# Kernel tuning notes

Hardware: AMD Instinct MI355X
Metric: run time of the kernel (lower is better)

## Reference

```python
import jax, jax.numpy as jnp
import numpy as np

B, D, H, E, TOPK = 65536, 1024, 512, 8, 2
LN_EPS = 1e-5
LB_WEIGHT = 0.01


def setup_inputs() -> dict:
    key = jax.random.key(0)
    ks = jax.random.split(key, 5)
    x = jax.random.normal(ks[0], (B, D), dtype=jnp.float32)
    W1 = jax.random.normal(ks[1], (D, H), dtype=jnp.float32) * 0.02
    b1 = jnp.zeros((H,), dtype=jnp.float32)
    ln_w = jnp.ones((H,), dtype=jnp.float32)
    ln_b = jnp.zeros((H,), dtype=jnp.float32)
    W2 = jax.random.normal(ks[2], (H, E), dtype=jnp.float32) * 0.02
    b2 = jnp.zeros((E,), dtype=jnp.float32)
    return {"x": x, "W1": W1, "b1": b1, "ln_w": ln_w, "ln_b": ln_b, "W2": W2, "b2": b2}


def _gate_logits(x, W1, b1, ln_w, ln_b, W2, b2):
    h = x @ W1 + b1                     # [B, H]
    mu = jnp.mean(h, axis=-1, keepdims=True)
    var = jnp.mean(jnp.square(h - mu), axis=-1, keepdims=True)
    h = (h - mu) * jax.lax.rsqrt(var + LN_EPS) * ln_w + ln_b
    h = jax.nn.gelu(h, approximate=False)  # torch nn.GELU default = exact erf
    return h @ W2 + b2                  # [B, E]


def reference(x, W1, b1, ln_w, ln_b, W2, b2):
    logits = _gate_logits(x, W1, b1, ln_w, ln_b, W2, b2)
    # sparse top-K routing (eval mode: no exploration noise)
    vals, idx = jax.lax.top_k(logits, TOPK)           # [B, K]
    rows = jnp.arange(logits.shape[0])[:, None]
    sparse = jnp.full_like(logits, -jnp.inf).at[rows, idx].set(vals)
    weights = jax.nn.softmax(sparse, axis=-1)         # zeros off top-k
    # Switch-style load-balance loss
    f = (weights > 0).astype(weights.dtype).mean(axis=0)  # fraction routed per expert
    P = weights.mean(axis=0)                              # mean gate prob per expert
    lb_loss = LB_WEIGHT * (E * jnp.sum(f * P))
    return weights, lb_loss
```

## Files before the change

kernel.cpp:

```cpp
#include <hip/hip_runtime.h>
#include <cstdint>
#include <cstddef>


typedef _Float16 f16;
typedef _Float16 f16x4 __attribute__((ext_vector_type(4)));
typedef _Float16 f16x8 __attribute__((ext_vector_type(8)));
typedef float f32x4 __attribute__((ext_vector_type(4)));

#define B_ROWS 65536
#define D_DIM 1024
#define H_DIM 512
#define E_DIM 8
#define BM 64
#define BK 32
#define THREADS 512
#define NCHUNK 32
#define LDPX 40
#define SLABH 2560
#define BUFH 5120
#define IMG_CH (H_DIM * BK)
#define IMG_TOTAL (32 * IMG_CH)
#define GACC_OFF ((size_t)2 * IMG_TOTAL * sizeof(f16))

__global__ void prep_split(const float* __restrict__ W1,
                           f16* __restrict__ wh, f16* __restrict__ wl) {
  int id = blockIdx.x * 256 + threadIdx.x;
  int h = id & (H_DIM - 1);
  int kg = id >> 9;
  int c = kg >> 2;
  int kk0 = (kg & 3) * 8;
  int k0 = kg * 8;
  f16x8 hv, lv;
#pragma unroll
  for (int j = 0; j < 8; ++j) {
    float v = W1[(size_t)(k0 + j) * H_DIM + h] * 64.0f;
    f16 hi = (f16)v;
    hv[j] = hi;
    lv[j] = (f16)((v - (float)hi) * 256.0f);
  }
  size_t o = (size_t)c * IMG_CH + (size_t)h * BK + kk0;
  *(f16x8*)&wh[o] = hv;
  *(f16x8*)&wl[o] = lv;
}

__global__ void zero_acc(float* __restrict__ acc) {
  if (threadIdx.x < 16) acc[threadIdx.x] = 0.0f;
}

__global__ __launch_bounds__(THREADS, 4) void fused_main(
    const float* __restrict__ x,
    const f16* __restrict__ wh, const f16* __restrict__ wl,
    const float* __restrict__ b1, const float* __restrict__ lnw,
    const float* __restrict__ lnb, const float* __restrict__ W2,
    const float* __restrict__ b2, float* __restrict__ out,
    float* __restrict__ gacc) {
  __shared__ __align__(16) char pool[45632];
  f16* sx = (f16*)pool;

  const int tid = threadIdx.x;
  const int lane = tid & 63;
  const int wv = tid >> 6;
  const int l15 = lane & 15;
  const int l4 = lane >> 4;
  const int64_t row0 = (int64_t)blockIdx.x * BM;

  const int srow = tid >> 3;
  const int sc4 = (tid & 7) * 4;
  const int swo = srow * LDPX + sc4;
  const float* xbase = x + (row0 + srow) * D_DIM + sc4;

  const f16* whp = wh + (wv * 64 + l15) * BK + l4 * 8;

  f32x4 acc[4][4];
#pragma unroll
  for (int m = 0; m < 4; ++m)
#pragma unroll
    for (int n = 0; n < 4; ++n) acc[m][n] = (f32x4){0.f, 0.f, 0.f, 0.f};

  f16x8 setB[2][4];

#define ISSUE(si, C, half)                                                    \
  do {                                                                        \
    const f16* p = whp + (size_t)((C) & 31) * IMG_CH + (half) * 1024;         \
    setB[si][0] = *(const f16x8*)(p);                                         \
    setB[si][1] = *(const f16x8*)(p + 512);                                   \
    setB[si][2] = *(const f16x8*)(p + IMG_TOTAL);                             \
    setB[si][3] = *(const f16x8*)(p + IMG_TOTAL + 512);                       \
  } while (0)

#define CHUNK_HALF(si, nh, bufv)                                              \
  do {                                                                        \
    __builtin_amdgcn_s_setprio(1);                                            \
    _Pragma("unroll") for (int m = 0; m < 4; ++m) {                           \
      const int ao = (bufv)*BUFH + (m * 16 + l15) * LDPX + l4 * 8;            \
      f16x8 ah = *(const f16x8*)&sx[ao];                                      \
      f16x8 al = *(const f16x8*)&sx[ao + SLABH];                              \
      f16x8 ahs;                                                              \
      _Pragma("unroll") for (int q = 0; q < 8; ++q) ahs[q] =                  \
          ah[q] * (f16)0.00390625f;                                           \
      acc[m][(nh)*2 + 0] = __builtin_amdgcn_mfma_f32_16x16x32_f16(            \
          ah, setB[si][0], acc[m][(nh)*2 + 0], 0, 0, 0);                      \
      acc[m][(nh)*2 + 0] = __builtin_amdgcn_mfma_f32_16x16x32_f16(            \
          al, setB[si][0], acc[m][(nh)*2 + 0], 0, 0, 0);                      \
      acc[m][(nh)*2 + 0] = __builtin_amdgcn_mfma_f32_16x16x32_f16(            \
          ahs, setB[si][2], acc[m][(nh)*2 + 0], 0, 0, 0);                     \
      acc[m][(nh)*2 + 1] = __builtin_amdgcn_mfma_f32_16x16x32_f16(            \
          ah, setB[si][1], acc[m][(nh)*2 + 1], 0, 0, 0);                      \
      acc[m][(nh)*2 + 1] = __builtin_amdgcn_mfma_f32_16x16x32_f16(            \
          al, setB[si][1], acc[m][(nh)*2 + 1], 0, 0, 0);                      \
      acc[m][(nh)*2 + 1] = __builtin_amdgcn_mfma_f32_16x16x32_f16(            \
          ahs, setB[si][3], acc[m][(nh)*2 + 1], 0, 0, 0);                     \
    }                                                                         \
    __builtin_amdgcn_s_setprio(0);                                            \
  } while (0)

#define WRITE_SLAB(bufv)                                                      \
  do {                                                                        \
    float vv[4] = {xv.x, xv.y, xv.z, xv.w};                                   \
    f16x4 hv, lv;                                                             \
    _Pragma("unroll") for (int q = 0; q < 4; ++q) {                           \
      float t = vv[q] * 64.0f;                                                \
      f16 hh = (f16)t;                                                        \
      hv[q] = hh;                                                             \
      lv[q] = (f16)(t - (float)hh);                                           \
    }                                                                         \
    *(f16x4*)&sx[(bufv)*BUFH + swo] = hv;                                     \
    *(f16x4*)&sx[(bufv)*BUFH + SLABH + swo] = lv;                             \
  } while (0)

#define SLAB_BARRIER()                                                        \
  do {                                                                        \
    asm volatile("s_waitcnt lgkmcnt(0)" ::: "memory");                        \
    __builtin_amdgcn_s_barrier();                                             \
    __builtin_amdgcn_sched_barrier(0);                                        \
  } while (0)

  float4 xv = *(const float4*)(xbase);
  WRITE_SLAB(0);
  ISSUE(0, 0, 0);
  ISSUE(1, 0, 1);
  xv = *(const float4*)(xbase + 32);
  SLAB_BARRIER();

  for (int c = 0; c < NCHUNK; ++c) {
    const int buf = c & 1;
    CHUNK_HALF(0, 0, buf);
    ISSUE(0, c + 1, 0);
    CHUNK_HALF(1, 1, buf);
    ISSUE(1, c + 1, 1);
    WRITE_SLAB(buf ^ 1);
    xv = *(const float4*)(xbase + ((c + 2) & 31) * 32);
    SLAB_BARRIER();
  }
#undef ISSUE
#undef CHUNK_HALF
#undef WRITE_SLAB
#undef SLAB_BARRIER
  __syncthreads();

  float* eW2T = (float*)pool;
  float* eStat = (float*)(pool + 24576);
  float* eLog = (float*)(pool + 28672);
  float* eMu = (float*)(pool + 45056);
  float* eRs = (float*)(pool + 45312);
  float* eFP = (float*)(pool + 45568);

  {
    float4 wa = *(const float4*)&W2[tid * 8];
    float4 wb = *(const float4*)&W2[tid * 8 + 4];
    *(float4*)&eW2T[tid * 12] = wa;
    *(float4*)&eW2T[tid * 12 + 4] = wb;
  }
  if (tid < 16) eFP[tid] = 0.0f;

  float bb[4], lw[4], lb[4];
#pragma unroll
  for (int n = 0; n < 4; ++n) {
    int col = wv * 64 + n * 16 + l15;
    bb[n] = b1[col] * 4096.0f;
    lw[n] = lnw[col];
    lb[n] = lnb[col];
#pragma unroll
    for (int m = 0; m < 4; ++m)
#pragma unroll
      for (int r = 0; r < 4; ++r) acc[m][n][r] += bb[n];
  }

#pragma unroll
  for (int m = 0; m < 4; ++m) {
    float s1[4] = {0, 0, 0, 0};
    float s2[4] = {0, 0, 0, 0};
#pragma unroll
    for (int n = 0; n < 4; ++n)
#pragma unroll
      for (int r = 0; r < 4; ++r) {
        float vv = acc[m][n][r];
        s1[r] += vv;
        s2[r] = fmaf(vv, vv, s2[r]);
      }
#pragma unroll
    for (int d = 1; d < 16; d <<= 1)
#pragma unroll
      for (int r = 0; r < 4; ++r) {
        s1[r] += __shfl_xor(s1[r], d);
        s2[r] += __shfl_xor(s2[r], d);
      }
    if (l15 == 0) {
      int rb = m * 16 + l4 * 4;
#pragma unroll
      for (int r = 0; r < 4; ++r) {
        eStat[(wv * 64 + rb + r) * 2 + 0] = s1[r];
        eStat[(wv * 64 + rb + r) * 2 + 1] = s2[r];
      }
    }
  }
  __syncthreads();
  if (tid < BM) {
    float s1 = 0.0f, s2 = 0.0f;
#pragma unroll
    for (int w = 0; w < 8; ++w) {
      s1 += eStat[(w * 64 + tid) * 2 + 0];
      s2 += eStat[(w * 64 + tid) * 2 + 1];
    }
    float mu = s1 * (1.0f / 512.0f);
    float var = s2 * (1.0f / 512.0f) - mu * mu;
    eMu[tid] = mu;
    eRs[tid] = 1.0f / sqrtf(var + (1e-5f * 4096.0f * 4096.0f));
  }
  __syncthreads();

#pragma unroll
  for (int m = 0; m < 4; ++m) {
    int rb = m * 16 + l4 * 4;
#pragma unroll
    for (int r = 0; r < 4; ++r) {
      float mu_r = eMu[rb + r];
      float rs_r = eRs[rb + r];
      float lg[8];
#pragma unroll
      for (int e = 0; e < 8; ++e) lg[e] = 0.0f;
#pragma unroll
      for (int n = 0; n < 4; ++n) {
        int col = wv * 64 + n * 16 + l15;
        float hn = (acc[m][n][r] - mu_r) * rs_r;
        float y = fmaf(hn, lw[n], lb[n]);
        float g = 0.5f * y * (1.0f + erff(y * 0.70710678118654752440f));
        float4 w0 = *(const float4*)&eW2T[col * 12];
        float4 w1 = *(const float4*)&eW2T[col * 12 + 4];
        lg[0] = fmaf(g, w0.x, lg[0]);
        lg[1] = fmaf(g, w0.y, lg[1]);
        lg[2] = fmaf(g, w0.z, lg[2]);
        lg[3] = fmaf(g, w0.w, lg[3]);
        lg[4] = fmaf(g, w1.x, lg[4]);
        lg[5] = fmaf(g, w1.y, lg[5]);
        lg[6] = fmaf(g, w1.z, lg[6]);
        lg[7] = fmaf(g, w1.w, lg[7]);
      }
#pragma unroll
      for (int d = 1; d < 16; d <<= 1)
#pragma unroll
        for (int e = 0; e < 8; ++e) lg[e] += __shfl_xor(lg[e], d);
      if (l15 == 0) {
#pragma unroll
        for (int e = 0; e < 8; ++e) eLog[(wv * 64 + rb + r) * 8 + e] = lg[e];
      }
    }
  }
  __syncthreads();

  if (tid < BM) {
    float v[8];
#pragma unroll
    for (int e = 0; e < 8; ++e) {
      float s = b2[e];
#pragma unroll
      for (int w = 0; w < 8; ++w) s += eLog[(w * 64 + tid) * 8 + e];
      v[e] = s;
    }
    float m1 = v[0];
    int i1 = 0;
#pragma unroll
    for (int e = 1; e < 8; ++e)
      if (v[e] > m1) { m1 = v[e]; i1 = e; }
    float m2 = -3.0e38f;
    int i2 = -1;
#pragma unroll
    for (int e = 0; e < 8; ++e)
      if (e != i1 && v[e] > m2) { m2 = v[e]; i2 = e; }
    float dd = expf(m2 - m1);
    float inv = 1.0f / (1.0f + dd);
    float wA = inv, wB = dd * inv;
    float o[8];
#pragma unroll
    for (int e = 0; e < 8; ++e)
      o[e] = (e == i1) ? wA : ((e == i2) ? wB : 0.0f);
    float4* op = (float4*)&out[(row0 + tid) * 8];
    op[0] = (float4){o[0], o[1], o[2], o[3]};
    op[1] = (float4){o[4], o[5], o[6], o[7]};
    atomicAdd(&eFP[i1], 1.0f);
    atomicAdd(&eFP[i2], 1.0f);
    atomicAdd(&eFP[8 + i1], wA);
    atomicAdd(&eFP[8 + i2], wB);
  }
  __syncthreads();
  if (tid < 16) atomicAdd(&gacc[tid], eFP[tid]);
}

__global__ void lb_final(const float* __restrict__ gacc, float* __restrict__ out) {
  if (threadIdx.x == 0) {
    const float invB = 1.0f / 65536.0f;
    float s = 0.0f;
#pragma unroll
    for (int e = 0; e < 8; ++e) s += (gacc[e] * invB) * (gacc[8 + e] * invB);
    out[(size_t)B_ROWS * E_DIM] = 0.01f * 8.0f * s;
  }
}

extern "C" void kernel_launch(void* const* d_in, const int* in_sizes, int n_in,
                              void* d_out, int out_size, void* d_ws, size_t ws_size,
                              hipStream_t stream) {
  (void)in_sizes; (void)n_in; (void)out_size; (void)ws_size;
  const float* x = (const float*)d_in[0];
  const float* W1 = (const float*)d_in[1];
  const float* b1 = (const float*)d_in[2];
  const float* lnw = (const float*)d_in[3];
  const float* lnb = (const float*)d_in[4];
  const float* W2 = (const float*)d_in[5];
  const float* b2 = (const float*)d_in[6];
  float* out = (float*)d_out;
  f16* wh = (f16*)d_ws;
  f16* wl = wh + IMG_TOTAL;
  float* gacc = (float*)((char*)d_ws + GACC_OFF);

  zero_acc<<<1, 64, 0, stream>>>(gacc);
  prep_split<<<(D_DIM * H_DIM / 8) / 256, 256, 0, stream>>>(W1, wh, wl);
  fused_main<<<B_ROWS / BM, THREADS, 0, stream>>>(x, wh, wl, b1, lnw, lnb, W2, b2,
                                                  out, gacc);
  lb_final<<<1, 64, 0, stream>>>(gacc, out);
}
```

Before: 249.7 us.

## Switch GEMM to 32x32x16 MFMA tiles with matching weight layout and epilogue

Replaces the 16x16x32 MFMA tiling with 32x32x16 MFMA instructions, so each wave holds 2x2 accumulator tiles of 16 floats. The weight image is re-laid out in K-steps of 16, and each 32-wide chunk is split into two k-steps. The epilogue is rewritten for the new accumulator row and column mapping, and it keeps W2 in registers instead of staging it in LDS, which shrinks LDS use. The goal is fewer MFMA and operand-load instructions per FLOP and higher occupancy from the smaller LDS footprint. In exchange, the epilogue needs longer 32-lane shuffle reductions.

```diff
diff --git a/kernel.cpp b/kernel.cpp
--- a/kernel.cpp
+++ b/kernel.cpp
@@ -6,7 +6,7 @@
 typedef _Float16 f16;
 typedef _Float16 f16x4 __attribute__((ext_vector_type(4)));
 typedef _Float16 f16x8 __attribute__((ext_vector_type(8)));
-typedef float f32x4 __attribute__((ext_vector_type(4)));
+typedef float f32x16 __attribute__((ext_vector_type(16)));
 
 #define B_ROWS 65536
 #define D_DIM 1024
@@ -19,8 +19,8 @@
 #define LDPX 40
 #define SLABH 2560
 #define BUFH 5120
-#define IMG_CH (H_DIM * BK)
-#define IMG_TOTAL (32 * IMG_CH)
+#define STEPH (H_DIM * 16)
+#define IMG_TOTAL (64 * STEPH)
 #define GACC_OFF ((size_t)2 * IMG_TOTAL * sizeof(f16))
 
 __global__ void prep_split(const float* __restrict__ W1,
@@ -28,9 +28,9 @@
   int id = blockIdx.x * 256 + threadIdx.x;
   int h = id & (H_DIM - 1);
   int kg = id >> 9;
-  int c = kg >> 2;
-  int kk0 = (kg & 3) * 8;
   int k0 = kg * 8;
+  int s = k0 >> 4;
+  int ko = k0 & 15;
   f16x8 hv, lv;
 #pragma unroll
   for (int j = 0; j < 8; ++j) {
@@ -39,7 +39,7 @@
     hv[j] = hi;
     lv[j] = (f16)((v - (float)hi) * 256.0f);
   }
-  size_t o = (size_t)c * IMG_CH + (size_t)h * BK + kk0;
+  size_t o = (size_t)s * STEPH + (size_t)h * 16 + ko;
   *(f16x8*)&wh[o] = hv;
   *(f16x8*)&wl[o] = lv;
 }
@@ -55,14 +55,14 @@
     const float* __restrict__ lnb, const float* __restrict__ W2,
     const float* __restrict__ b2, float* __restrict__ out,
     float* __restrict__ gacc) {
-  __shared__ __align__(16) char pool[45632];
+  __shared__ __align__(16) char pool[21056];
   f16* sx = (f16*)pool;
 
   const int tid = threadIdx.x;
   const int lane = tid & 63;
   const int wv = tid >> 6;
-  const int l15 = lane & 15;
-  const int l4 = lane >> 4;
+  const int l31 = lane & 31;
+  const int hi5 = lane >> 5;
   const int64_t row0 = (int64_t)blockIdx.x * BM;
 
   const int srow = tid >> 3;
@@ -70,47 +70,50 @@
   const int swo = srow * LDPX + sc4;
   const float* xbase = x + (row0 + srow) * D_DIM + sc4;
 
-  const f16* whp = wh + (wv * 64 + l15) * BK + l4 * 8;
-
-  f32x4 acc[4][4];
-#pragma unroll
-  for (int m = 0; m < 4; ++m)
-#pragma unroll
-    for (int n = 0; n < 4; ++n) acc[m][n] = (f32x4){0.f, 0.f, 0.f, 0.f};
+  const int blane = (wv * 64 + l31) * 16 + hi5 * 8;
+  const f16* whp = wh + blane;
+
+  f32x16 acc[2][2];
+#pragma unroll
+  for (int mt = 0; mt < 2; ++mt)
+#pragma unroll
+    for (int nt = 0; nt < 2; ++nt)
+#pragma unroll
+      for (int r = 0; r < 16; ++r) acc[mt][nt][r] = 0.0f;
 
   f16x8 setB[2][4];
 
-#define ISSUE(si, C, half)                                                    \
+#define ISSUE(si, G)                                                          \
   do {                                                                        \
-    const f16* p = whp + (size_t)((C) & 31) * IMG_CH + (half) * 1024;         \
+    const f16* p = whp + (size_t)((G) & 63) * STEPH;                          \
     setB[si][0] = *(const f16x8*)(p);                                         \
     setB[si][1] = *(const f16x8*)(p + 512);                                   \
     setB[si][2] = *(const f16x8*)(p + IMG_TOTAL);                             \
     setB[si][3] = *(const f16x8*)(p + IMG_TOTAL + 512);                       \
   } while (0)
 
-#define CHUNK_HALF(si, nh, bufv)                                              \
+#define KSTEP(si, ks, bufv)                                                   \
   do {                                                                        \
     __builtin_amdgcn_s_setprio(1);                                            \
-    _Pragma("unroll") for (int m = 0; m < 4; ++m) {                           \
-      const int ao = (bufv)*BUFH + (m * 16 + l15) * LDPX + l4 * 8;            \
+    _Pragma("unroll") for (int mt = 0; mt < 2; ++mt) {                        \
+      const int ao = (bufv)*BUFH + (mt * 32 + l31) * LDPX + (ks)*16 + hi5 * 8;\
       f16x8 ah = *(const f16x8*)&sx[ao];                                      \
       f16x8 al = *(const f16x8*)&sx[ao + SLABH];                              \
       f16x8 ahs;                                                              \
       _Pragma("unroll") for (int q = 0; q < 8; ++q) ahs[q] =                  \
           ah[q] * (f16)0.00390625f;                                           \
-      acc[m][(nh)*2 + 0] = __builtin_amdgcn_mfma_f32_16x16x32_f16(            \
-          ah, setB[si][0], acc[m][(nh)*2 + 0], 0, 0, 0);                      \
-      acc[m][(nh)*2 + 0] = __builtin_amdgcn_mfma_f32_16x16x32_f16(            \
-          al, setB[si][0], acc[m][(nh)*2 + 0], 0, 0, 0);                      \
-      acc[m][(nh)*2 + 0] = __builtin_amdgcn_mfma_f32_16x16x32_f16(            \
-          ahs, setB[si][2], acc[m][(nh)*2 + 0], 0, 0, 0);                     \
-      acc[m][(nh)*2 + 1] = __builtin_amdgcn_mfma_f32_16x16x32_f16(            \
-          ah, setB[si][1], acc[m][(nh)*2 + 1], 0, 0, 0);                      \
-      acc[m][(nh)*2 + 1] = __builtin_amdgcn_mfma_f32_16x16x32_f16(            \
-          al, setB[si][1], acc[m][(nh)*2 + 1], 0, 0, 0);                      \
-      acc[m][(nh)*2 + 1] = __builtin_amdgcn_mfma_f32_16x16x32_f16(            \
-          ahs, setB[si][3], acc[m][(nh)*2 + 1], 0, 0, 0);                     \
+      acc[mt][0] = __builtin_amdgcn_mfma_f32_32x32x16_f16(                    \
+          ah, setB[si][0], acc[mt][0], 0, 0, 0);                              \
+      acc[mt][0] = __builtin_amdgcn_mfma_f32_32x32x16_f16(                    \
+          al, setB[si][0], acc[mt][0], 0, 0, 0);                              \
+      acc[mt][0] = __builtin_amdgcn_mfma_f32_32x32x16_f16(                    \
+          ahs, setB[si][2], acc[mt][0], 0, 0, 0);                             \
+      acc[mt][1] = __builtin_amdgcn_mfma_f32_32x32x16_f16(                    \
+          ah, setB[si][1], acc[mt][1], 0, 0, 0);                              \
+      acc[mt][1] = __builtin_amdgcn_mfma_f32_32x32x16_f16(                    \
+          al, setB[si][1], acc[mt][1], 0, 0, 0);                              \
+      acc[mt][1] = __builtin_amdgcn_mfma_f32_32x32x16_f16(                    \
+          ahs, setB[si][3], acc[mt][1], 0, 0, 0);                             \
     }                                                                         \
     __builtin_amdgcn_s_setprio(0);                                            \
   } while (0)
@@ -138,83 +141,81 @@
 
   float4 xv = *(const float4*)(xbase);
   WRITE_SLAB(0);
-  ISSUE(0, 0, 0);
-  ISSUE(1, 0, 1);
+  ISSUE(0, 0);
+  ISSUE(1, 1);
   xv = *(const float4*)(xbase + 32);
   SLAB_BARRIER();
 
   for (int c = 0; c < NCHUNK; ++c) {
     const int buf = c & 1;
-    CHUNK_HALF(0, 0, buf);
-    ISSUE(0, c + 1, 0);
-    CHUNK_HALF(1, 1, buf);
-    ISSUE(1, c + 1, 1);
+    KSTEP(0, 0, buf);
+    ISSUE(0, 2 * c + 2);
+    KSTEP(1, 1, buf);
+    ISSUE(1, 2 * c + 3);
     WRITE_SLAB(buf ^ 1);
     xv = *(const float4*)(xbase + ((c + 2) & 31) * 32);
     SLAB_BARRIER();
   }
 #undef ISSUE
-#undef CHUNK_HALF
+#undef KSTEP
 #undef WRITE_SLAB
 #undef SLAB_BARRIER
   __syncthreads();
 
-  float* eW2T = (float*)pool;
-  float* eStat = (float*)(pool + 24576);
-  float* eLog = (float*)(pool + 28672);
-  float* eMu = (float*)(pool + 45056);
-  float* eRs = (float*)(pool + 45312);
-  float* eFP = (float*)(pool + 45568);
-
-  {
-    float4 wa = *(const float4*)&W2[tid * 8];
-    float4 wb = *(const float4*)&W2[tid * 8 + 4];
-    *(float4*)&eW2T[tid * 12] = wa;
-    *(float4*)&eW2T[tid * 12 + 4] = wb;
+  float* eStat = (float*)pool;
+  float* eLog = (float*)(pool + 4096);
+  float* eMu = (float*)(pool + 20480);
+  float* eRs = (float*)(pool + 20736);
+  float* eFP = (float*)(pool + 20992);
+
+  float bb[2], lw[2], lb[2];
+  float4 w2a[2], w2b[2];
+#pragma unroll
+  for (int nt = 0; nt < 2; ++nt) {
+    int col = wv * 64 + nt * 32 + l31;
+    bb[nt] = b1[col] * 4096.0f;
+    lw[nt] = lnw[col];
+    lb[nt] = lnb[col];
+    w2a[nt] = *(const float4*)&W2[col * 8];
+    w2b[nt] = *(const float4*)&W2[col * 8 + 4];
   }
   if (tid < 16) eFP[tid] = 0.0f;
 
-  float bb[4], lw[4], lb[4];
-#pragma unroll
-  for (int n = 0; n < 4; ++n) {
-    int col = wv * 64 + n * 16 + l15;
-    bb[n] = b1[col] * 4096.0f;
-    lw[n] = lnw[col];
-    lb[n] = lnb[col];
-#pragma unroll
-    for (int m = 0; m < 4; ++m)
-#pragma unroll
-      for (int r = 0; r < 4; ++r) acc[m][n][r] += bb[n];
-  }
-
-#pragma unroll
-  for (int m = 0; m < 4; ++m) {
-    float s1[4] = {0, 0, 0, 0};
-    float s2[4] = {0, 0, 0, 0};
-#pragma unroll
-    for (int n = 0; n < 4; ++n)
+#pragma unroll
+  for (int mt = 0; mt < 2; ++mt)
+#pragma unroll
+    for (int nt = 0; nt < 2; ++nt)
+#pragma unroll
+      for (int r = 0; r < 16; ++r) acc[mt][nt][r] += bb[nt];
+
+#pragma unroll
+  for (int mt = 0; mt < 2; ++mt)
+#pragma unroll
+    for (int q = 0; q < 4; ++q) {
+      float s1[4], s2[4];
 #pragma unroll
       for (int r = 0; r < 4; ++r) {
-        float vv = acc[m][n][r];
-        s1[r] += vv;
-        s2[r] = fmaf(vv, vv, s2[r]);
+        float v0 = acc[mt][0][q * 4 + r];
+        float v1 = acc[mt][1][q * 4 + r];
+        s1[r] = v0 + v1;
+        s2[r] = fmaf(v0, v0, v1 * v1);
       }
 #pragma unroll
-    for (int d = 1; d < 16; d <<= 1)
-#pragma unroll
-      for (int r = 0; r < 4; ++r) {
-        s1[r] += __shfl_xor(s1[r], d);
-        s2[r] += __shfl_xor(s2[r], d);
-      }
-    if (l15 == 0) {
-      int rb = m * 16 + l4 * 4;
-#pragma unroll
-      for (int r = 0; r < 4; ++r) {
-        eStat[(wv * 64 + rb + r) * 2 + 0] = s1[r];
-        eStat[(wv * 64 + rb + r) * 2 + 1] = s2[r];
+      for (int d = 1; d < 32; d <<= 1)
+#pragma unroll
+        for (int r = 0; r < 4; ++r) {
+          s1[r] += __shfl_xor(s1[r], d);
+          s2[r] += __shfl_xor(s2[r], d);
+        }
+      if (l31 == 0) {
+        int rb = 8 * q + 4 * hi5 + 32 * mt;
+#pragma unroll
+        for (int r = 0; r < 4; ++r) {
+          eStat[(wv * 64 + rb + r) * 2 + 0] = s1[r];
+          eStat[(wv * 64 + rb + r) * 2 + 1] = s2[r];
+        }
       }
     }
-  }
   __syncthreads();
   if (tid < BM) {
     float s1 = 0.0f, s2 = 0.0f;
@@ -231,42 +232,41 @@
   __syncthreads();
 
 #pragma unroll
-  for (int m = 0; m < 4; ++m) {
-    int rb = m * 16 + l4 * 4;
-#pragma unroll
-    for (int r = 0; r < 4; ++r) {
-      float mu_r = eMu[rb + r];
-      float rs_r = eRs[rb + r];
-      float lg[8];
-#pragma unroll
-      for (int e = 0; e < 8; ++e) lg[e] = 0.0f;
-#pragma unroll
-      for (int n = 0; n < 4; ++n) {
-        int col = wv * 64 + n * 16 + l15;
-        float hn = (acc[m][n][r] - mu_r) * rs_r;
-        float y = fmaf(hn, lw[n], lb[n]);
-        float g = 0.5f * y * (1.0f + erff(y * 0.70710678118654752440f));
-        float4 w0 = *(const float4*)&eW2T[col * 12];
-        float4 w1 = *(const float4*)&eW2T[col * 12 + 4];
-        lg[0] = fmaf(g, w0.x, lg[0]);
-        lg[1] = fmaf(g, w0.y, lg[1]);
-        lg[2] = fmaf(g, w0.z, lg[2]);
-        lg[3] = fmaf(g, w0.w, lg[3]);
-        lg[4] = fmaf(g, w1.x, lg[4]);
-        lg[5] = fmaf(g, w1.y, lg[5]);
-        lg[6] = fmaf(g, w1.z, lg[6]);
-        lg[7] = fmaf(g, w1.w, lg[7]);
+  for (int mt = 0; mt < 2; ++mt)
+#pragma unroll
+    for (int q = 0; q < 4; ++q)
+#pragma unroll
+      for (int r = 0; r < 4; ++r) {
+        const int reg = q * 4 + r;
+        const int row = r + 8 * q + 4 * hi5 + 32 * mt;
+        float mu_r = eMu[row];
+        float rs_r = eRs[row];
+        float lg[8];
+#pragma unroll
+        for (int e = 0; e < 8; ++e) lg[e] = 0.0f;
+#pragma unroll
+        for (int nt = 0; nt < 2; ++nt) {
+          float hn = (acc[mt][nt][reg] - mu_r) * rs_r;
+          float y = fmaf(hn, lw[nt], lb[nt]);
+          float g = 0.5f * y * (1.0f + erff(y * 0.70710678118654752440f));
+          lg[0] = fmaf(g, w2a[nt].x, lg[0]);
+          lg[1] = fmaf(g, w2a[nt].y, lg[1]);
+          lg[2] = fmaf(g, w2a[nt].z, lg[2]);
+          lg[3] = fmaf(g, w2a[nt].w, lg[3]);
+          lg[4] = fmaf(g, w2b[nt].x, lg[4]);
+          lg[5] = fmaf(g, w2b[nt].y, lg[5]);
+          lg[6] = fmaf(g, w2b[nt].z, lg[6]);
+          lg[7] = fmaf(g, w2b[nt].w, lg[7]);
+        }
+#pragma unroll
+        for (int d = 1; d < 32; d <<= 1)
+#pragma unroll
+          for (int e = 0; e < 8; ++e) lg[e] += __shfl_xor(lg[e], d);
+        if (l31 == 0) {
+#pragma unroll
+          for (int e = 0; e < 8; ++e) eLog[(wv * 64 + row) * 8 + e] = lg[e];
+        }
       }
-#pragma unroll
-      for (int d = 1; d < 16; d <<= 1)
-#pragma unroll
-        for (int e = 0; e < 8; ++e) lg[e] += __shfl_xor(lg[e], d);
-      if (l15 == 0) {
-#pragma unroll
-        for (int e = 0; e < 8; ++e) eLog[(wv * 64 + rb + r) * 8 + e] = lg[e];
-      }
-    }
-  }
   __syncthreads();
 
   if (tid < BM) {
```

Result: slower. 315.1 us (+26.2%).

## Stage 64-wide K super-chunks in LDS to halve barriers per K loop

Applied to the files above, without the earlier changes.

Each shared-memory slab now holds 64 K columns instead of 32. Each thread loads two float4s and writes 8-wide f16 hi/lo vectors, and the main loop runs 16 super-iterations of two 32-wide sub-chunks, so the barrier and slab-write overhead is paid half as often. The MFMA sequence is also interleaved across the two accumulators to ease dependency stalls. The cost is more LDS per block (padded stride 72), which may lower occupancy under the 4-block launch bound, and the weight register prefetch still advances per 32-chunk.

```diff
diff --git a/kernel.cpp b/kernel.cpp
--- a/kernel.cpp
+++ b/kernel.cpp
@@ -4,7 +4,6 @@
 
 
 typedef _Float16 f16;
-typedef _Float16 f16x4 __attribute__((ext_vector_type(4)));
 typedef _Float16 f16x8 __attribute__((ext_vector_type(8)));
 typedef float f32x4 __attribute__((ext_vector_type(4)));
 
@@ -15,10 +14,10 @@
 #define BM 64
 #define BK 32
 #define THREADS 512
-#define NCHUNK 32
-#define LDPX 40
-#define SLABH 2560
-#define BUFH 5120
+#define NSUPER 16
+#define LDPX 72
+#define SLABH 4608
+#define BUFH 9216
 #define IMG_CH (H_DIM * BK)
 #define IMG_TOTAL (32 * IMG_CH)
 #define GACC_OFF ((size_t)2 * IMG_TOTAL * sizeof(f16))
@@ -66,9 +65,9 @@
   const int64_t row0 = (int64_t)blockIdx.x * BM;
 
   const int srow = tid >> 3;
-  const int sc4 = (tid & 7) * 4;
-  const int swo = srow * LDPX + sc4;
-  const float* xbase = x + (row0 + srow) * D_DIM + sc4;
+  const int sk = (tid & 7) * 8;
+  const int swo = srow * LDPX + sk;
+  const float* xbase = x + (row0 + srow) * D_DIM + sk;
 
   const f16* whp = wh + (wv * 64 + l15) * BK + l4 * 8;
 
@@ -89,11 +88,11 @@
     setB[si][3] = *(const f16x8*)(p + IMG_TOTAL + 512);                       \
   } while (0)
 
-#define CHUNK_HALF(si, nh, bufv)                                              \
+#define CHUNK_HALF(si, nh, ch, bufv)                                          \
   do {                                                                        \
     __builtin_amdgcn_s_setprio(1);                                            \
     _Pragma("unroll") for (int m = 0; m < 4; ++m) {                           \
-      const int ao = (bufv)*BUFH + (m * 16 + l15) * LDPX + l4 * 8;            \
+      const int ao = (bufv)*BUFH + (m * 16 + l15) * LDPX + (ch)*32 + l4 * 8;  \
       f16x8 ah = *(const f16x8*)&sx[ao];                                      \
       f16x8 al = *(const f16x8*)&sx[ao + SLABH];                              \
       f16x8 ahs;                                                              \
@@ -101,14 +100,14 @@
           ah[q] * (f16)0.00390625f;                                           \
       acc[m][(nh)*2 + 0] = __builtin_amdgcn_mfma_f32_16x16x32_f16(            \
           ah, setB[si][0], acc[m][(nh)*2 + 0], 0, 0, 0);                      \
+      acc[m][(nh)*2 + 1] = __builtin_amdgcn_mfma_f32_16x16x32_f16(            \
+          ah, setB[si][1], acc[m][(nh)*2 + 1], 0, 0, 0);                      \
       acc[m][(nh)*2 + 0] = __builtin_amdgcn_mfma_f32_16x16x32_f16(            \
           al, setB[si][0], acc[m][(nh)*2 + 0], 0, 0, 0);                      \
+      acc[m][(nh)*2 + 1] = __builtin_amdgcn_mfma_f32_16x16x32_f16(            \
+          al, setB[si][1], acc[m][(nh)*2 + 1], 0, 0, 0);                      \
       acc[m][(nh)*2 + 0] = __builtin_amdgcn_mfma_f32_16x16x32_f16(            \
           ahs, setB[si][2], acc[m][(nh)*2 + 0], 0, 0, 0);                     \
-      acc[m][(nh)*2 + 1] = __builtin_amdgcn_mfma_f32_16x16x32_f16(            \
-          ah, setB[si][1], acc[m][(nh)*2 + 1], 0, 0, 0);                      \
-      acc[m][(nh)*2 + 1] = __builtin_amdgcn_mfma_f32_16x16x32_f16(            \
-          al, setB[si][1], acc[m][(nh)*2 + 1], 0, 0, 0);                      \
       acc[m][(nh)*2 + 1] = __builtin_amdgcn_mfma_f32_16x16x32_f16(            \
           ahs, setB[si][3], acc[m][(nh)*2 + 1], 0, 0, 0);                     \
     }                                                                         \
@@ -117,16 +116,16 @@
 
 #define WRITE_SLAB(bufv)                                                      \
   do {                                                                        \
-    float vv[4] = {xv.x, xv.y, xv.z, xv.w};                                   \
-    f16x4 hv, lv;                                                             \
-    _Pragma("unroll") for (int q = 0; q < 4; ++q) {                           \
+    float vv[8] = {xv0.x, xv0.y, xv0.z, xv0.w, xv1.x, xv1.y, xv1.z, xv1.w};   \
+    f16x8 hv, lv;                                                             \
+    _Pragma("unroll") for (int q = 0; q < 8; ++q) {                           \
       float t = vv[q] * 64.0f;                                                \
       f16 hh = (f16)t;                                                        \
       hv[q] = hh;                                                             \
       lv[q] = (f16)(t - (float)hh);                                           \
     }                                                                         \
-    *(f16x4*)&sx[(bufv)*BUFH + swo] = hv;                                     \
-    *(f16x4*)&sx[(bufv)*BUFH + SLABH + swo] = lv;                             \
+    *(f16x8*)&sx[(bufv)*BUFH + swo] = hv;                                     \
+    *(f16x8*)&sx[(bufv)*BUFH + SLABH + swo] = lv;                             \
   } while (0)
 
 #define SLAB_BARRIER()                                                        \
@@ -136,21 +135,28 @@
     __builtin_amdgcn_sched_barrier(0);                                        \
   } while (0)
 
-  float4 xv = *(const float4*)(xbase);
+  float4 xv0 = *(const float4*)(xbase);
+  float4 xv1 = *(const float4*)(xbase + 4);
   WRITE_SLAB(0);
   ISSUE(0, 0, 0);
   ISSUE(1, 0, 1);
-  xv = *(const float4*)(xbase + 32);
+  xv0 = *(const float4*)(xbase + 64);
+  xv1 = *(const float4*)(xbase + 68);
   SLAB_BARRIER();
 
-  for (int c = 0; c < NCHUNK; ++c) {
-    const int buf = c & 1;
-    CHUNK_HALF(0, 0, buf);
-    ISSUE(0, c + 1, 0);
-    CHUNK_HALF(1, 1, buf);
-    ISSUE(1, c + 1, 1);
+  for (int s = 0; s < NSUPER; ++s) {
+    const int buf = s & 1;
+    CHUNK_HALF(0, 0, 0, buf);
+    ISSUE(0, 2 * s + 1, 0);
+    CHUNK_HALF(1, 1, 0, buf);
+    ISSUE(1, 2 * s + 1, 1);
+    CHUNK_HALF(0, 0, 1, buf);
+    ISSUE(0, 2 * s + 2, 0);
+    CHUNK_HALF(1, 1, 1, buf);
+    ISSUE(1, 2 * s + 2, 1);
     WRITE_SLAB(buf ^ 1);
-    xv = *(const float4*)(xbase + ((c + 2) & 31) * 32);
+    xv0 = *(const float4*)(xbase + (((s + 2) & 15) * 64));
+    xv1 = *(const float4*)(xbase + (((s + 2) & 15) * 64) + 4);
     SLAB_BARRIER();
   }
 #undef ISSUE
```

Result: no change. 248.9 us (-0.3%).

## Halve block to 4 waves, each computing 128 H columns per row tile

Applied to the files above, without the earlier changes.

The block shrinks from 8 waves to 4. Each wave now owns 128 hidden columns (8 accumulator tiles) instead of 64, so every A-fragment read from LDS feeds twice as many MFMAs and B loads are issued 8 per half-chunk. The x staging load widens to two float4s per thread, and the cross-wave reductions for LN stats and logits shrink to 4 waves. In exchange, register pressure roughly doubles (acc[4][8] plus setB[2][8]), launch bounds drop to 2 blocks, and there are fewer waves to hide global-load latency.

```diff
diff --git a/kernel.cpp b/kernel.cpp
--- a/kernel.cpp
+++ b/kernel.cpp
@@ -4,7 +4,6 @@
 
 
 typedef _Float16 f16;
-typedef _Float16 f16x4 __attribute__((ext_vector_type(4)));
 typedef _Float16 f16x8 __attribute__((ext_vector_type(8)));
 typedef float f32x4 __attribute__((ext_vector_type(4)));
 
@@ -14,7 +13,7 @@
 #define E_DIM 8
 #define BM 64
 #define BK 32
-#define THREADS 512
+#define THREADS 256
 #define NCHUNK 32
 #define LDPX 40
 #define SLABH 2560
@@ -48,14 +47,14 @@
   if (threadIdx.x < 16) acc[threadIdx.x] = 0.0f;
 }
 
-__global__ __launch_bounds__(THREADS, 4) void fused_main(
+__global__ __launch_bounds__(THREADS, 2) void fused_main(
     const float* __restrict__ x,
     const f16* __restrict__ wh, const f16* __restrict__ wl,
     const float* __restrict__ b1, const float* __restrict__ lnw,
     const float* __restrict__ lnb, const float* __restrict__ W2,
     const float* __restrict__ b2, float* __restrict__ out,
     float* __restrict__ gacc) {
-  __shared__ __align__(16) char pool[45632];
+  __shared__ __align__(16) char pool[35584];
   f16* sx = (f16*)pool;
 
   const int tid = threadIdx.x;
@@ -65,68 +64,75 @@
   const int l4 = lane >> 4;
   const int64_t row0 = (int64_t)blockIdx.x * BM;
 
-  const int srow = tid >> 3;
-  const int sc4 = (tid & 7) * 4;
-  const int swo = srow * LDPX + sc4;
-  const float* xbase = x + (row0 + srow) * D_DIM + sc4;
-
-  const f16* whp = wh + (wv * 64 + l15) * BK + l4 * 8;
-
-  f32x4 acc[4][4];
+  const int srow = tid >> 2;
+  const int koff = (tid & 3) * 8;
+  const int swo = srow * LDPX + koff;
+  const float* xbase = x + (row0 + srow) * D_DIM + koff;
+
+  const f16* whp = wh + (wv * 128 + l15) * BK + l4 * 8;
+
+  f32x4 acc[4][8];
 #pragma unroll
   for (int m = 0; m < 4; ++m)
 #pragma unroll
-    for (int n = 0; n < 4; ++n) acc[m][n] = (f32x4){0.f, 0.f, 0.f, 0.f};
-
-  f16x8 setB[2][4];
+    for (int n = 0; n < 8; ++n) acc[m][n] = (f32x4){0.f, 0.f, 0.f, 0.f};
+
+  f16x8 setB[2][8];
 
 #define ISSUE(si, C, half)                                                    \
   do {                                                                        \
-    const f16* p = whp + (size_t)((C) & 31) * IMG_CH + (half) * 1024;         \
+    const f16* p = whp + (size_t)((C) & 31) * IMG_CH + (half) * 2048;         \
     setB[si][0] = *(const f16x8*)(p);                                         \
     setB[si][1] = *(const f16x8*)(p + 512);                                   \
-    setB[si][2] = *(const f16x8*)(p + IMG_TOTAL);                             \
-    setB[si][3] = *(const f16x8*)(p + IMG_TOTAL + 512);                       \
-  } while (0)
-
-#define CHUNK_HALF(si, nh, bufv)                                              \
+    setB[si][2] = *(const f16x8*)(p + 1024);                                  \
+    setB[si][3] = *(const f16x8*)(p + 1536);                                  \
+    setB[si][4] = *(const f16x8*)(p + IMG_TOTAL);                             \
+    setB[si][5] = *(const f16x8*)(p + IMG_TOTAL + 512);                       \
+    setB[si][6] = *(const f16x8*)(p + IMG_TOTAL + 1024);                      \
+    setB[si][7] = *(const f16x8*)(p + IMG_TOTAL + 1536);                      \
+  } while (0)
+
+#define CH_M(si, NH, bufv, MM)                                                \
+  do {                                                                        \
+    const int ao = (bufv)*BUFH + ((MM)*16 + l15) * LDPX + l4 * 8;             \
+    f16x8 ah = *(const f16x8*)&sx[ao];                                        \
+    f16x8 al = *(const f16x8*)&sx[ao + SLABH];                                \
+    f16x8 ahs;                                                                \
+    _Pragma("unroll") for (int q = 0; q < 8; ++q) ahs[q] =                    \
+        ah[q] * (f16)0.00390625f;                                             \
+    _Pragma("unroll") for (int n = 0; n < 4; ++n)                             \
+      acc[MM][(NH)*4 + n] = __builtin_amdgcn_mfma_f32_16x16x32_f16(           \
+          ah, setB[si][n], acc[MM][(NH)*4 + n], 0, 0, 0);                     \
+    _Pragma("unroll") for (int n = 0; n < 4; ++n)                             \
+      acc[MM][(NH)*4 + n] = __builtin_amdgcn_mfma_f32_16x16x32_f16(           \
+          al, setB[si][n], acc[MM][(NH)*4 + n], 0, 0, 0);                     \
+    _Pragma("unroll") for (int n = 0; n < 4; ++n)                             \
+      acc[MM][(NH)*4 + n] = __builtin_amdgcn_mfma_f32_16x16x32_f16(           \
+          ahs, setB[si][4 + n], acc[MM][(NH)*4 + n], 0, 0, 0);                \
+  } while (0)
+
+#define HALF(si, NH, bufv)                                                    \
   do {                                                                        \
     __builtin_amdgcn_s_setprio(1);                                            \
-    _Pragma("unroll") for (int m = 0; m < 4; ++m) {                           \
-      const int ao = (bufv)*BUFH + (m * 16 + l15) * LDPX + l4 * 8;            \
-      f16x8 ah = *(const f16x8*)&sx[ao];                                      \
-      f16x8 al = *(const f16x8*)&sx[ao + SLABH];                              \
-      f16x8 ahs;                                                              \
-      _Pragma("unroll") for (int q = 0; q < 8; ++q) ahs[q] =                  \
-          ah[q] * (f16)0.00390625f;                                           \
-      acc[m][(nh)*2 + 0] = __builtin_amdgcn_mfma_f32_16x16x32_f16(            \
-          ah, setB[si][0], acc[m][(nh)*2 + 0], 0, 0, 0);                      \
-      acc[m][(nh)*2 + 0] = __builtin_amdgcn_mfma_f32_16x16x32_f16(            \
-          al, setB[si][0], acc[m][(nh)*2 + 0], 0, 0, 0);                      \
-      acc[m][(nh)*2 + 0] = __builtin_amdgcn_mfma_f32_16x16x32_f16(            \
-          ahs, setB[si][2], acc[m][(nh)*2 + 0], 0, 0, 0);                     \
-      acc[m][(nh)*2 + 1] = __builtin_amdgcn_mfma_f32_16x16x32_f16(            \
-          ah, setB[si][1], acc[m][(nh)*2 + 1], 0, 0, 0);                      \
-      acc[m][(nh)*2 + 1] = __builtin_amdgcn_mfma_f32_16x16x32_f16(            \
-          al, setB[si][1], acc[m][(nh)*2 + 1], 0, 0, 0);                      \
-      acc[m][(nh)*2 + 1] = __builtin_amdgcn_mfma_f32_16x16x32_f16(            \
-          ahs, setB[si][3], acc[m][(nh)*2 + 1], 0, 0, 0);                     \
-    }                                                                         \
+    CH_M(si, NH, bufv, 0);                                                    \
+    CH_M(si, NH, bufv, 1);                                                    \
+    CH_M(si, NH, bufv, 2);                                                    \
+    CH_M(si, NH, bufv, 3);                                                    \
     __builtin_amdgcn_s_setprio(0);                                            \
   } while (0)
 
 #define WRITE_SLAB(bufv)                                                      \
   do {                                                                        \
-    float vv[4] = {xv.x, xv.y, xv.z, xv.w};                                   \
-    f16x4 hv, lv;                                                             \
-    _Pragma("unroll") for (int q = 0; q < 4; ++q) {                           \
+    float vv[8] = {xv0.x, xv0.y, xv0.z, xv0.w, xv1.x, xv1.y, xv1.z, xv1.w};   \
+    f16x8 hv, lv;                                                             \
+    _Pragma("unroll") for (int q = 0; q < 8; ++q) {                           \
       float t = vv[q] * 64.0f;                                                \
       f16 hh = (f16)t;                                                        \
       hv[q] = hh;                                                             \
       lv[q] = (f16)(t - (float)hh);                                           \
     }                                                                         \
-    *(f16x4*)&sx[(bufv)*BUFH + swo] = hv;                                     \
-    *(f16x4*)&sx[(bufv)*BUFH + SLABH + swo] = lv;                             \
+    *(f16x8*)&sx[(bufv)*BUFH + swo] = hv;                                     \
+    *(f16x8*)&sx[(bufv)*BUFH + SLABH + swo] = lv;                             \
   } while (0)
 
 #define SLAB_BARRIER()                                                        \
@@ -136,48 +142,52 @@
     __builtin_amdgcn_sched_barrier(0);                                        \
   } while (0)
 
-  float4 xv = *(const float4*)(xbase);
+  float4 xv0 = *(const float4*)(xbase);
+  float4 xv1 = *(const float4*)(xbase + 4);
   WRITE_SLAB(0);
   ISSUE(0, 0, 0);
   ISSUE(1, 0, 1);
-  xv = *(const float4*)(xbase + 32);
+  xv0 = *(const float4*)(xbase + 32);
+  xv1 = *(const float4*)(xbase + 36);
   SLAB_BARRIER();
 
   for (int c = 0; c < NCHUNK; ++c) {
     const int buf = c & 1;
-    CHUNK_HALF(0, 0, buf);
+    HALF(0, 0, buf);
     ISSUE(0, c + 1, 0);
-    CHUNK_HALF(1, 1, buf);
+    HALF(1, 1, buf);
     ISSUE(1, c + 1, 1);
     WRITE_SLAB(buf ^ 1);
-    xv = *(const float4*)(xbase + ((c + 2) & 31) * 32);
+    xv0 = *(const float4*)(xbase + ((c + 2) & 31) * 32);
+    xv1 = *(const float4*)(xbase + ((c + 2) & 31) * 32 + 4);
     SLAB_BARRIER();
   }
 #undef ISSUE
-#undef CHUNK_HALF
+#undef CH_M
+#undef HALF
 #undef WRITE_SLAB
 #undef SLAB_BARRIER
   __syncthreads();
 
   float* eW2T = (float*)pool;
   float* eStat = (float*)(pool + 24576);
-  float* eLog = (float*)(pool + 28672);
-  float* eMu = (float*)(pool + 45056);
-  float* eRs = (float*)(pool + 45312);
-  float* eFP = (float*)(pool + 45568);
-
-  {
-    float4 wa = *(const float4*)&W2[tid * 8];
-    float4 wb = *(const float4*)&W2[tid * 8 + 4];
-    *(float4*)&eW2T[tid * 12] = wa;
-    *(float4*)&eW2T[tid * 12 + 4] = wb;
+  float* eLog = (float*)(pool + 26624);
+  float* eMu = (float*)(pool + 34816);
+  float* eRs = (float*)(pool + 35072);
+  float* eFP = (float*)(pool + 35328);
+
+  for (int i = tid; i < H_DIM; i += THREADS) {
+    float4 wa = *(const float4*)&W2[i * 8];
+    float4 wb = *(const float4*)&W2[i * 8 + 4];
+    *(float4*)&eW2T[i * 12] = wa;
+    *(float4*)&eW2T[i * 12 + 4] = wb;
   }
   if (tid < 16) eFP[tid] = 0.0f;
 
-  float bb[4], lw[4], lb[4];
-#pragma unroll
-  for (int n = 0; n < 4; ++n) {
-    int col = wv * 64 + n * 16 + l15;
+  float bb[8], lw[8], lb[8];
+#pragma unroll
+  for (int n = 0; n < 8; ++n) {
+    int col = wv * 128 + n * 16 + l15;
     bb[n] = b1[col] * 4096.0f;
     lw[n] = lnw[col];
     lb[n] = lnb[col];
@@ -192,7 +202,7 @@
     float s1[4] = {0, 0, 0, 0};
     float s2[4] = {0, 0, 0, 0};
 #pragma unroll
-    for (int n = 0; n < 4; ++n)
+    for (int n = 0; n < 8; ++n)
 #pragma unroll
       for (int r = 0; r < 4; ++r) {
         float vv = acc[m][n][r];
@@ -219,7 +229,7 @@
   if (tid < BM) {
     float s1 = 0.0f, s2 = 0.0f;
 #pragma unroll
-    for (int w = 0; w < 8; ++w) {
+    for (int w = 0; w < 4; ++w) {
       s1 += eStat[(w * 64 + tid) * 2 + 0];
       s2 += eStat[(w * 64 + tid) * 2 + 1];
     }
@@ -241,8 +251,8 @@
 #pragma unroll
       for (int e = 0; e < 8; ++e) lg[e] = 0.0f;
 #pragma unroll
-      for (int n = 0; n < 4; ++n) {
-        int col = wv * 64 + n * 16 + l15;
+      for (int n = 0; n < 8; ++n) {
+        int col = wv * 128 + n * 16 + l15;
         float hn = (acc[m][n][r] - mu_r) * rs_r;
         float y = fmaf(hn, lw[n], lb[n]);
         float g = 0.5f * y * (1.0f + erff(y * 0.70710678118654752440f));
@@ -275,7 +285,7 @@
     for (int e = 0; e < 8; ++e) {
       float s = b2[e];
 #pragma unroll
-      for (int w = 0; w < 8; ++w) s += eLog[(w * 64 + tid) * 8 + e];
+      for (int w = 0; w < 4; ++w) s += eLog[(w * 64 + tid) * 8 + e];
       v[e] = s;
     }
     float m1 = v[0];
```

Measured after the change: 242.4 us. -2.9%, faster.
